# Performance work log

Hardware: AMD Instinct MI355X
Metric: run time of the kernel (lower is better)

## Reference

```python
import jax, jax.numpy as jnp
import numpy as np

B, L, X, Y, A = 32, 1024, 1024, 1024, 16


def setup_inputs() -> dict:
    key = jax.random.key(0)
    ks = jax.random.split(key, 6)
    stdv = 1.0 / np.sqrt(X)
    stdv_h = 1.0 / np.sqrt(Y)
    return {
        "x": jax.random.normal(ks[0], (B, L, X), dtype=jnp.float32),
        "y": jax.random.normal(ks[1], (B, Y), dtype=jnp.float32),
        "x_mask": jnp.zeros((B, L), dtype=bool),
        "actions": jax.random.randint(ks[2], (B,), 0, A),
        "weight": jax.random.uniform(ks[3], (Y, X), minval=-stdv, maxval=stdv, dtype=jnp.float32),
        "bias": jnp.zeros((X,), dtype=jnp.float32),
        "wa_h": jax.random.uniform(ks[4], (A, Y, 1), minval=-stdv_h, maxval=stdv_h, dtype=jnp.float32),
    }


def reference(x, y, x_mask, actions, weight, bias, wa_h):
    # Per-action column scores: softmax over x_size of sum_y(weight * wa_h[a])
    # (equivalent to the torch loop: a2 = weight*wa_h[a]; softmax(a2.sum(0)))
    score2 = jax.nn.softmax(jnp.einsum("yx,ay->ax", weight, wa_h[:, :, 0]), axis=-1)  # [A, X]
    # u[b,a,:] = y[b] @ (weight * score2[a]) = (y@weight)[b] * score2[a];
    # the one-hot mask then selects row actions[b] -> gather instead of A GEMMs.
    yW = y @ weight                                   # [B, X]
    Wy = yW * score2[actions] + bias                  # [B, X]
    xWy = jnp.einsum("blx,bx->bl", x, Wy)             # [B, L]
    xWy = jnp.where(x_mask, -jnp.inf, xWy)
    return jax.nn.log_softmax(xWy, axis=-1)  # training mode
```

## Files before the change

kernel.cpp:

```cpp
#include <hip/hip_runtime.h>
#include <hip/hip_bf16.h>
#include <math.h>

constexpr int Ac = 16;
constexpr int Bc = 32;
constexpr int Lc = 1024;
constexpr int Xc = 1024;
constexpr int Yc = 1024;
constexpr int Cc = Ac + Bc;

typedef float vfloat4 __attribute__((ext_vector_type(4)));

__device__ __forceinline__ float waveReduceSum(float v) {
#pragma unroll
    for (int off = 32; off > 0; off >>= 1) v += __shfl_down(v, off, 64);
    return v;
}

__device__ __forceinline__ float waveReduceMax(float v) {
#pragma unroll
    for (int off = 32; off > 0; off >>= 1) v = fmaxf(v, __shfl_down(v, off, 64));
    return v;
}

__global__ __launch_bounds__(256) void k1_proj(
        const float* __restrict__ weight, const float* __restrict__ yv,
        const float* __restrict__ wa_h, float* __restrict__ s_raw,
        float* __restrict__ yW) {
    const int x  = blockIdx.x * 256 + threadIdx.x;
    const int y0 = blockIdx.y * 32;

    __shared__ float cLDS[Cc][32];

#pragma unroll
    for (int k = 0; k < 6; ++k) {
        const int idx = threadIdx.x + k * 256;
        const int row = idx >> 5;
        const int col = idx & 31;
        cLDS[row][col] = (row < Ac) ? wa_h[row * Yc + y0 + col]
                                    : yv[(row - Ac) * Yc + y0 + col];
    }

    float w[32];
#pragma unroll
    for (int t = 0; t < 32; ++t) w[t] = weight[(size_t)(y0 + t) * Xc + x];

    __syncthreads();

    float acc[Cc];
#pragma unroll
    for (int j = 0; j < Cc; ++j) acc[j] = 0.0f;

    const float4* cvec = (const float4*)cLDS;
#pragma unroll
    for (int j = 0; j < Cc; ++j) {
#pragma unroll
        for (int q = 0; q < 8; ++q) {
            const float4 c = cvec[j * 8 + q];
            acc[j] = fmaf(w[q * 4 + 0], c.x, acc[j]);
            acc[j] = fmaf(w[q * 4 + 1], c.y, acc[j]);
            acc[j] = fmaf(w[q * 4 + 2], c.z, acc[j]);
            acc[j] = fmaf(w[q * 4 + 3], c.w, acc[j]);
        }
    }

#pragma unroll
    for (int j = 0; j < Ac; ++j) atomicAdd(&s_raw[j * Xc + x], acc[j]);
#pragma unroll
    for (int j = Ac; j < Cc; ++j) atomicAdd(&yW[(j - Ac) * Xc + x], acc[j]);
}

__global__ __launch_bounds__(256) void k2_softmax(
        const float* __restrict__ s_raw, float* __restrict__ score2) {
    const int a    = blockIdx.x;
    const int tid  = threadIdx.x;
    const int wave = tid >> 6;
    const int lane = tid & 63;
    __shared__ float smax[4];
    __shared__ float ssum[4];

    float v[4];
    float mx = -INFINITY;
#pragma unroll
    for (int k = 0; k < 4; ++k) {
        v[k] = s_raw[a * Xc + tid + k * 256];
        mx = fmaxf(mx, v[k]);
    }
    mx = waveReduceMax(mx);
    if (lane == 0) smax[wave] = mx;
    __syncthreads();
    mx = fmaxf(fmaxf(smax[0], smax[1]), fmaxf(smax[2], smax[3]));

    float sum = 0.0f;
#pragma unroll
    for (int k = 0; k < 4; ++k) {
        v[k] = __expf(v[k] - mx);
        sum += v[k];
    }
    sum = waveReduceSum(sum);
    if (lane == 0) ssum[wave] = sum;
    __syncthreads();
    sum = ssum[0] + ssum[1] + ssum[2] + ssum[3];

    const float inv = 1.0f / sum;
#pragma unroll
    for (int k = 0; k < 4; ++k) score2[a * Xc + tid + k * 256] = v[k] * inv;
}

__global__ __launch_bounds__(256) void k3_dot(
        const float* __restrict__ x, const float* __restrict__ yW,
        const float* __restrict__ score2, const float* __restrict__ bias,
        const int* __restrict__ actions, float* __restrict__ xWy) {
    const int b  = blockIdx.y;
    const int l0 = blockIdx.x * 16;
    __shared__ float Wy[Xc];

    const int act = actions[b];
#pragma unroll
    for (int k = 0; k < 4; ++k) {
        const int xi = threadIdx.x + k * 256;
        Wy[xi] = fmaf(yW[b * Xc + xi], score2[act * Xc + xi], bias[xi]);
    }
    __syncthreads();

    const int wave = threadIdx.x >> 6;
    const int lane = threadIdx.x & 63;
    const float4* WyV = (const float4*)Wy;

    for (int r = wave; r < 16; r += 4) {
        const int l = l0 + r;
        const vfloat4* xp = (const vfloat4*)(x + ((size_t)b * Lc + l) * Xc);
        float acc = 0.0f;
#pragma unroll
        for (int k = 0; k < 4; ++k) {
            const int idx = lane + k * 64;
            const vfloat4 xv = __builtin_nontemporal_load(&xp[idx]);
            const float4 wv = WyV[idx];
            acc = fmaf(xv.x, wv.x, acc);
            acc = fmaf(xv.y, wv.y, acc);
            acc = fmaf(xv.z, wv.z, acc);
            acc = fmaf(xv.w, wv.w, acc);
        }
        acc = waveReduceSum(acc);
        if (lane == 0) xWy[b * Lc + l] = acc;
    }
}

__global__ __launch_bounds__(256) void k4_logsoftmax(
        const float* __restrict__ xWy, const unsigned char* __restrict__ mask,
        float* __restrict__ out) {
    const int b    = blockIdx.x;
    const int tid  = threadIdx.x;
    const int wave = tid >> 6;
    const int lane = tid & 63;
    __shared__ float smax[4];
    __shared__ float ssum[4];

    float v[4];
    float mx = -INFINITY;
#pragma unroll
    for (int k = 0; k < 4; ++k) {
        const int l = tid + k * 256;
        float t = xWy[b * Lc + l];
        if (mask[b * Lc + l]) t = -INFINITY;
        v[k] = t;
        mx = fmaxf(mx, t);
    }
    mx = waveReduceMax(mx);
    if (lane == 0) smax[wave] = mx;
    __syncthreads();
    mx = fmaxf(fmaxf(smax[0], smax[1]), fmaxf(smax[2], smax[3]));

    float sum = 0.0f;
#pragma unroll
    for (int k = 0; k < 4; ++k) sum += __expf(v[k] - mx);
    sum = waveReduceSum(sum);
    if (lane == 0) ssum[wave] = sum;
    __syncthreads();
    sum = ssum[0] + ssum[1] + ssum[2] + ssum[3];

    const float lse = mx + __logf(sum);
#pragma unroll
    for (int k = 0; k < 4; ++k) out[b * Lc + tid + k * 256] = v[k] - lse;
}

extern "C" void kernel_launch(void* const* d_in, const int* in_sizes, int n_in,
                              void* d_out, int out_size, void* d_ws, size_t ws_size,
                              hipStream_t stream) {
    const float* x          = (const float*)d_in[0];
    const float* yv         = (const float*)d_in[1];
    const unsigned char* xm = (const unsigned char*)d_in[2];
    const int* actions      = (const int*)d_in[3];
    const float* weight     = (const float*)d_in[4];
    const float* bias       = (const float*)d_in[5];
    const float* wa_h       = (const float*)d_in[6];
    float* out              = (float*)d_out;

    char* ws      = (char*)d_ws;
    float* s_raw  = (float*)(ws);
    float* yW     = (float*)(ws + 64 * 1024);
    float* score2 = (float*)(ws + 192 * 1024);
    float* xWy    = (float*)(ws + 256 * 1024);

    (void)hipMemsetAsync(d_ws, 0, 192 * 1024, stream);

    k1_proj<<<dim3(Xc / 256, Yc / 32), 256, 0, stream>>>(weight, yv, wa_h, s_raw, yW);
    k2_softmax<<<Ac, 256, 0, stream>>>(s_raw, score2);
    k3_dot<<<dim3(Lc / 16, Bc), 256, 0, stream>>>(x, yW, score2, bias, actions, xWy);
    k4_logsoftmax<<<Bc, 256, 0, stream>>>(xWy, xm, out);
}
```

Baseline: 213.2 us.

## Fuse softmax into projection and log-softmax into dot kernel via atomic counters

Merges the per-action softmax into the projection kernel: every block bumps a global counter, and the first 16 blocks spin until all blocks have finished before computing softmax rows. The log-softmax is folded into the dot kernel with a last-block-per-batch pattern driven by per-batch counters. This removes two kernel launches and their inter-kernel gaps. In exchange it adds fences, atomics and a spin-wait that assumes every block of the 128-block grid is co-resident.

```diff
diff --git a/kernel.cpp b/kernel.cpp
--- a/kernel.cpp
+++ b/kernel.cpp
@@ -1,5 +1,4 @@
 #include <hip/hip_runtime.h>
-#include <hip/hip_bf16.h>
 #include <math.h>
 
 constexpr int Ac = 16;
@@ -23,10 +22,11 @@
     return v;
 }
 
-__global__ __launch_bounds__(256) void k1_proj(
+__global__ __launch_bounds__(256) void k1_proj_sm(
         const float* __restrict__ weight, const float* __restrict__ yv,
         const float* __restrict__ wa_h, float* __restrict__ s_raw,
-        float* __restrict__ yW) {
+        float* __restrict__ yW, float* __restrict__ score2,
+        unsigned* __restrict__ cnt) {
     const int x  = blockIdx.x * 256 + threadIdx.x;
     const int y0 = blockIdx.y * 32;
 
@@ -68,11 +68,23 @@
     for (int j = 0; j < Ac; ++j) atomicAdd(&s_raw[j * Xc + x], acc[j]);
 #pragma unroll
     for (int j = Ac; j < Cc; ++j) atomicAdd(&yW[(j - Ac) * Xc + x], acc[j]);
-}
-
-__global__ __launch_bounds__(256) void k2_softmax(
-        const float* __restrict__ s_raw, float* __restrict__ score2) {
-    const int a    = blockIdx.x;
+
+    __threadfence();
+    __syncthreads();
+    if (threadIdx.x == 0) atomicAdd(cnt, 1u);
+
+    const int fid = blockIdx.y * gridDim.x + blockIdx.x;
+    if (fid >= Ac) return;
+
+    const unsigned total = gridDim.x * gridDim.y;
+    if (threadIdx.x == 0) {
+        while (__hip_atomic_load(cnt, __ATOMIC_ACQUIRE,
+                                 __HIP_MEMORY_SCOPE_AGENT) < total)
+            __builtin_amdgcn_s_sleep(2);
+    }
+    __syncthreads();
+
+    const int a    = fid;
     const int tid  = threadIdx.x;
     const int wave = tid >> 6;
     const int lane = tid & 63;
@@ -83,7 +95,8 @@
     float mx = -INFINITY;
 #pragma unroll
     for (int k = 0; k < 4; ++k) {
-        v[k] = s_raw[a * Xc + tid + k * 256];
+        v[k] = __hip_atomic_load(&s_raw[a * Xc + tid + k * 256],
+                                 __ATOMIC_RELAXED, __HIP_MEMORY_SCOPE_AGENT);
         mx = fmaxf(mx, v[k]);
     }
     mx = waveReduceMax(mx);
@@ -107,10 +120,12 @@
     for (int k = 0; k < 4; ++k) score2[a * Xc + tid + k * 256] = v[k] * inv;
 }
 
-__global__ __launch_bounds__(256) void k3_dot(
+__global__ __launch_bounds__(256) void k3_dot_lsm(
         const float* __restrict__ x, const float* __restrict__ yW,
         const float* __restrict__ score2, const float* __restrict__ bias,
-        const int* __restrict__ actions, float* __restrict__ xWy) {
+        const int* __restrict__ actions, const unsigned char* __restrict__ mask,
+        float* __restrict__ xWy, float* __restrict__ out,
+        unsigned* __restrict__ cnt3) {
     const int b  = blockIdx.y;
     const int l0 = blockIdx.x * 16;
     __shared__ float Wy[Xc];
@@ -144,15 +159,20 @@
         acc = waveReduceSum(acc);
         if (lane == 0) xWy[b * Lc + l] = acc;
     }
-}
-
-__global__ __launch_bounds__(256) void k4_logsoftmax(
-        const float* __restrict__ xWy, const unsigned char* __restrict__ mask,
-        float* __restrict__ out) {
-    const int b    = blockIdx.x;
+
+    __threadfence();
+    __syncthreads();
+    __shared__ int lastFlag;
+    if (threadIdx.x == 0) {
+        const unsigned old = atomicAdd(&cnt3[b], 1u);
+        lastFlag = (old == gridDim.x - 1);
+    }
+    __syncthreads();
+    if (!lastFlag) return;
+
     const int tid  = threadIdx.x;
-    const int wave = tid >> 6;
-    const int lane = tid & 63;
+    const int wv   = tid >> 6;
+    const int ln   = tid & 63;
     __shared__ float smax[4];
     __shared__ float ssum[4];
 
@@ -161,13 +181,14 @@
 #pragma unroll
     for (int k = 0; k < 4; ++k) {
         const int l = tid + k * 256;
-        float t = xWy[b * Lc + l];
+        float t = __hip_atomic_load(&xWy[b * Lc + l], __ATOMIC_RELAXED,
+                                    __HIP_MEMORY_SCOPE_AGENT);
         if (mask[b * Lc + l]) t = -INFINITY;
         v[k] = t;
         mx = fmaxf(mx, t);
     }
     mx = waveReduceMax(mx);
-    if (lane == 0) smax[wave] = mx;
+    if (ln == 0) smax[wv] = mx;
     __syncthreads();
     mx = fmaxf(fmaxf(smax[0], smax[1]), fmaxf(smax[2], smax[3]));
 
@@ -175,7 +196,7 @@
 #pragma unroll
     for (int k = 0; k < 4; ++k) sum += __expf(v[k] - mx);
     sum = waveReduceSum(sum);
-    if (lane == 0) ssum[wave] = sum;
+    if (ln == 0) ssum[wv] = sum;
     __syncthreads();
     sum = ssum[0] + ssum[1] + ssum[2] + ssum[3];
 
@@ -196,16 +217,18 @@
     const float* wa_h       = (const float*)d_in[6];
     float* out              = (float*)d_out;
 
-    char* ws      = (char*)d_ws;
-    float* s_raw  = (float*)(ws);
-    float* yW     = (float*)(ws + 64 * 1024);
-    float* score2 = (float*)(ws + 192 * 1024);
-    float* xWy    = (float*)(ws + 256 * 1024);
-
-    (void)hipMemsetAsync(d_ws, 0, 192 * 1024, stream);
-
-    k1_proj<<<dim3(Xc / 256, Yc / 32), 256, 0, stream>>>(weight, yv, wa_h, s_raw, yW);
-    k2_softmax<<<Ac, 256, 0, stream>>>(s_raw, score2);
-    k3_dot<<<dim3(Lc / 16, Bc), 256, 0, stream>>>(x, yW, score2, bias, actions, xWy);
-    k4_logsoftmax<<<Bc, 256, 0, stream>>>(xWy, xm, out);
-}
+    char* ws        = (char*)d_ws;
+    unsigned* cnt3  = (unsigned*)(ws);
+    unsigned* cnt1  = (unsigned*)(ws + 128);
+    float* s_raw    = (float*)(ws + 4 * 1024);
+    float* yW       = (float*)(ws + 68 * 1024);
+    float* score2   = (float*)(ws + 196 * 1024);
+    float* xWy      = (float*)(ws + 260 * 1024);
+
+    (void)hipMemsetAsync(d_ws, 0, 196 * 1024, stream);
+
+    k1_proj_sm<<<dim3(Xc / 256, Yc / 32), 256, 0, stream>>>(
+        weight, yv, wa_h, s_raw, yW, score2, cnt1);
+    k3_dot_lsm<<<dim3(Lc / 16, Bc), 256, 0, stream>>>(
+        x, yW, score2, bias, actions, xm, xWy, out, cnt3);
+}
```

Measured after the change: 527.4 us. 2.47x slower.

## Fuse per-action softmax into dot kernel and batch four rows per wave

Applied to the files above, without the earlier changes.

Removes the separate softmax kernel by having each dot block recompute the softmax of the selected action's score row, then build Wy in shared memory directly. The dot loop now issues four row loads per wave before the FMAs so more memory requests are in flight. This drops one launch and the score2 round trip, but every block (2048 of them) redundantly recomputes a 1024-element softmax with two extra barriers.

```diff
diff --git a/kernel.cpp b/kernel.cpp
--- a/kernel.cpp
+++ b/kernel.cpp
@@ -1,5 +1,4 @@
 #include <hip/hip_runtime.h>
-#include <hip/hip_bf16.h>
 #include <math.h>
 
 constexpr int Ac = 16;
@@ -70,21 +69,27 @@
     for (int j = Ac; j < Cc; ++j) atomicAdd(&yW[(j - Ac) * Xc + x], acc[j]);
 }
 
-__global__ __launch_bounds__(256) void k2_softmax(
-        const float* __restrict__ s_raw, float* __restrict__ score2) {
-    const int a    = blockIdx.x;
+__global__ __launch_bounds__(256) void k3_dot(
+        const float* __restrict__ x, const float* __restrict__ yW,
+        const float* __restrict__ s_raw, const float* __restrict__ bias,
+        const int* __restrict__ actions, float* __restrict__ xWy) {
+    const int b   = blockIdx.y;
+    const int l0  = blockIdx.x * 16;
     const int tid  = threadIdx.x;
     const int wave = tid >> 6;
     const int lane = tid & 63;
+    __shared__ float Wy[Xc];
     __shared__ float smax[4];
     __shared__ float ssum[4];
 
-    float v[4];
+    const int act = actions[b];
+
+    float sv[4];
     float mx = -INFINITY;
 #pragma unroll
     for (int k = 0; k < 4; ++k) {
-        v[k] = s_raw[a * Xc + tid + k * 256];
-        mx = fmaxf(mx, v[k]);
+        sv[k] = s_raw[act * Xc + tid + k * 256];
+        mx = fmaxf(mx, sv[k]);
     }
     mx = waveReduceMax(mx);
     if (lane == 0) smax[wave] = mx;
@@ -94,55 +99,49 @@
     float sum = 0.0f;
 #pragma unroll
     for (int k = 0; k < 4; ++k) {
-        v[k] = __expf(v[k] - mx);
-        sum += v[k];
+        sv[k] = __expf(sv[k] - mx);
+        sum += sv[k];
     }
     sum = waveReduceSum(sum);
     if (lane == 0) ssum[wave] = sum;
     __syncthreads();
     sum = ssum[0] + ssum[1] + ssum[2] + ssum[3];
-
     const float inv = 1.0f / sum;
-#pragma unroll
-    for (int k = 0; k < 4; ++k) score2[a * Xc + tid + k * 256] = v[k] * inv;
-}
-
-__global__ __launch_bounds__(256) void k3_dot(
-        const float* __restrict__ x, const float* __restrict__ yW,
-        const float* __restrict__ score2, const float* __restrict__ bias,
-        const int* __restrict__ actions, float* __restrict__ xWy) {
-    const int b  = blockIdx.y;
-    const int l0 = blockIdx.x * 16;
-    __shared__ float Wy[Xc];
-
-    const int act = actions[b];
-#pragma unroll
-    for (int k = 0; k < 4; ++k) {
-        const int xi = threadIdx.x + k * 256;
-        Wy[xi] = fmaf(yW[b * Xc + xi], score2[act * Xc + xi], bias[xi]);
-    }
-    __syncthreads();
-
-    const int wave = threadIdx.x >> 6;
-    const int lane = threadIdx.x & 63;
+
+#pragma unroll
+    for (int k = 0; k < 4; ++k) {
+        const int xi = tid + k * 256;
+        Wy[xi] = fmaf(yW[b * Xc + xi], sv[k] * inv, bias[xi]);
+    }
+    __syncthreads();
+
     const float4* WyV = (const float4*)Wy;
-
-    for (int r = wave; r < 16; r += 4) {
-        const int l = l0 + r;
-        const vfloat4* xp = (const vfloat4*)(x + ((size_t)b * Lc + l) * Xc);
-        float acc = 0.0f;
-#pragma unroll
-        for (int k = 0; k < 4; ++k) {
-            const int idx = lane + k * 64;
-            const vfloat4 xv = __builtin_nontemporal_load(&xp[idx]);
-            const float4 wv = WyV[idx];
-            acc = fmaf(xv.x, wv.x, acc);
-            acc = fmaf(xv.y, wv.y, acc);
-            acc = fmaf(xv.z, wv.z, acc);
-            acc = fmaf(xv.w, wv.w, acc);
+    const float* xb = x + ((size_t)b * Lc + l0) * Xc;
+
+    float acc[4] = {0.0f, 0.0f, 0.0f, 0.0f};
+#pragma unroll
+    for (int k = 0; k < 4; ++k) {
+        const int idx = lane + k * 64;
+        const float4 wv = WyV[idx];
+        vfloat4 xv[4];
+#pragma unroll
+        for (int rr = 0; rr < 4; ++rr) {
+            const int l = wave + rr * 4;
+            xv[rr] = __builtin_nontemporal_load(
+                (const vfloat4*)(xb + (size_t)l * Xc) + idx);
         }
-        acc = waveReduceSum(acc);
-        if (lane == 0) xWy[b * Lc + l] = acc;
+#pragma unroll
+        for (int rr = 0; rr < 4; ++rr) {
+            acc[rr] = fmaf(xv[rr].x, wv.x, acc[rr]);
+            acc[rr] = fmaf(xv[rr].y, wv.y, acc[rr]);
+            acc[rr] = fmaf(xv[rr].z, wv.z, acc[rr]);
+            acc[rr] = fmaf(xv[rr].w, wv.w, acc[rr]);
+        }
+    }
+#pragma unroll
+    for (int rr = 0; rr < 4; ++rr) {
+        const float a = waveReduceSum(acc[rr]);
+        if (lane == 0) xWy[b * Lc + l0 + wave + rr * 4] = a;
     }
 }
 
@@ -199,13 +198,11 @@
     char* ws      = (char*)d_ws;
     float* s_raw  = (float*)(ws);
     float* yW     = (float*)(ws + 64 * 1024);
-    float* score2 = (float*)(ws + 192 * 1024);
-    float* xWy    = (float*)(ws + 256 * 1024);
+    float* xWy    = (float*)(ws + 192 * 1024);
 
     (void)hipMemsetAsync(d_ws, 0, 192 * 1024, stream);
 
     k1_proj<<<dim3(Xc / 256, Yc / 32), 256, 0, stream>>>(weight, yv, wa_h, s_raw, yW);
-    k2_softmax<<<Ac, 256, 0, stream>>>(s_raw, score2);
-    k3_dot<<<dim3(Lc / 16, Bc), 256, 0, stream>>>(x, yW, score2, bias, actions, xWy);
+    k3_dot<<<dim3(Lc / 16, Bc), 256, 0, stream>>>(x, yW, s_raw, bias, actions, xWy);
     k4_logsoftmax<<<Bc, 256, 0, stream>>>(xWy, xm, out);
 }
```

New measurement: 211.5 us. No clear change (-0.8%).
